# Performance work log

Hardware: AMD Instinct MI355X
Metric: run time of the kernel (lower is better)

## Reference

```python
import jax, jax.numpy as jnp
import numpy as np

BINS = 32


def _mi_from_hist(hist):
    # hist: (B, BINS, BINS) raw counts. Normalize and compute MI per sample,
    # matching np.histogram2d marginals (px from axis=1 sum, py from axis=0 sum).
    total = jnp.sum(hist, axis=(1, 2), keepdims=True)
    p = hist / total                      # joint pmf (B, BINS, BINS)
    px = jnp.sum(p, axis=2)               # (B, BINS)
    py = jnp.sum(p, axis=1)               # (B, BINS)
    denom = px[:, :, None] * py[:, None, :]
    pos = p > 0                           # p>0 implies px>0 and py>0
    ratio = jnp.where(pos, p / jnp.where(pos, denom, 1.0), 1.0)
    mi = jnp.sum(jnp.where(pos, p * jnp.log(ratio), 0.0), axis=(1, 2))
    return mi                             # (B,)


def setup_inputs() -> dict:
    key = jax.random.key(0)
    k1, k2 = jax.random.split(key)
    shape = (32, 2, 512, 512)
    return {
        "input": jax.random.normal(k1, shape, dtype=jnp.float32),
        "target": jax.random.normal(k2, shape, dtype=jnp.float32),
    }


def reference(input, target):
    B = input.shape[0]
    u = (input.reshape(B, -1) + 1.0) / 2.0   # (B, N) mapped to ~[0,1]
    v = (target.reshape(B, -1) + 1.0) / 2.0
    # np.histogram2d with range [[0,1],[0,1]] drops out-of-range points and
    # includes the right edge in the last bin.
    in_range = (u >= 0) & (u <= 1) & (v >= 0) & (v <= 1)
    w = in_range.astype(u.dtype)
    iu = jnp.clip(jnp.floor(u * BINS).astype(jnp.int32), 0, BINS - 1)
    iv = jnp.clip(jnp.floor(v * BINS).astype(jnp.int32), 0, BINS - 1)
    flat = (jnp.arange(B, dtype=jnp.int32)[:, None] * (BINS * BINS)
            + iu * BINS + iv).reshape(-1)
    hist = jax.ops.segment_sum(w.reshape(-1), flat,
                               num_segments=B * BINS * BINS)
    hist = hist.reshape(B, BINS, BINS)
    mi = _mi_from_hist(hist)
    return -jnp.mean(mi)
```

## Files before the change

### kernel.cpp

```cpp
#include <hip/hip_runtime.h>


#define BINS 32
#define NBINS2 1024
#define LDS_ROW 33
#define LDS_HIST (BINS * LDS_ROW)
#define NBATCH 32
#define N_PER_BATCH (2 * 512 * 512)
#define BLOCKS_PER_BATCH 64
#define CHUNK (N_PER_BATCH / BLOCKS_PER_BATCH)
#define THREADS 256
#define VEC_PER_THREAD (CHUNK / 4 / THREADS)

__global__ __launch_bounds__(THREADS) void zero_kernel(unsigned* __restrict__ hist,
                                                       double* __restrict__ mi,
                                                       float* __restrict__ out) {
    int i = blockIdx.x * THREADS + threadIdx.x;
    if (i < NBATCH * NBINS2) hist[i] = 0u;
    if (i < NBATCH) mi[i] = 0.0;
    if (i == 0) out[0] = 0.0f;
}

__global__ __launch_bounds__(THREADS) void hist_kernel(const float* __restrict__ x,
                                                       const float* __restrict__ y,
                                                       unsigned* __restrict__ hist) {
    __shared__ unsigned h[LDS_HIST];
    for (int i = threadIdx.x; i < LDS_HIST; i += THREADS) h[i] = 0u;
    __syncthreads();

    const int b   = blockIdx.x / BLOCKS_PER_BATCH;
    const int blk = blockIdx.x % BLOCKS_PER_BATCH;
    const long base = (long)b * N_PER_BATCH + (long)blk * CHUNK;
    const float4* xv = (const float4*)(x + base);
    const float4* yv = (const float4*)(y + base);

    float4 xa[VEC_PER_THREAD], ya[VEC_PER_THREAD];
#pragma unroll
    for (int j = 0; j < VEC_PER_THREAD; ++j) xa[j] = xv[threadIdx.x + j * THREADS];
#pragma unroll
    for (int j = 0; j < VEC_PER_THREAD; ++j) ya[j] = yv[threadIdx.x + j * THREADS];

#pragma unroll
    for (int j = 0; j < VEC_PER_THREAD; ++j) {
        float ax[4] = {xa[j].x, xa[j].y, xa[j].z, xa[j].w};
        float ty[4] = {ya[j].x, ya[j].y, ya[j].z, ya[j].w};
#pragma unroll
        for (int k = 0; k < 4; ++k) {
            float u = (ax[k] + 1.0f) * 0.5f;
            float v = (ty[k] + 1.0f) * 0.5f;
            bool ok = (u >= 0.0f) & (u <= 1.0f) & (v >= 0.0f) & (v <= 1.0f);
            if (ok) {
                int iu = (int)(u * 32.0f); if (iu > 31) iu = 31;
                int iv = (int)(v * 32.0f); if (iv > 31) iv = 31;
                atomicAdd(&h[iu * LDS_ROW + iv], 1u);
            }
        }
    }
    __syncthreads();

    unsigned* g = hist + b * NBINS2;
    for (int i = threadIdx.x; i < NBINS2; i += THREADS) {
        unsigned v = h[(i >> 5) * LDS_ROW + (i & 31)];
        if (v) atomicAdd(&g[i], v);
    }
}

__global__ __launch_bounds__(256) void mi_kernel(const unsigned* __restrict__ hist,
                                                 double* __restrict__ mi_out) {
    __shared__ unsigned c[NBINS2];
    __shared__ unsigned px[BINS];
    __shared__ unsigned py[BINS];
    __shared__ double red[4];

    const int b = blockIdx.x;
    const unsigned* g = hist + b * NBINS2;
    for (int i = threadIdx.x; i < NBINS2; i += 256) c[i] = g[i];
    __syncthreads();

    if (threadIdx.x < 32) {
        unsigned s = 0;
        for (int j = 0; j < 32; ++j) s += c[threadIdx.x * BINS + j];
        px[threadIdx.x] = s;
    } else if (threadIdx.x < 64) {
        int col = threadIdx.x - 32;
        unsigned s = 0;
        for (int j = 0; j < 32; ++j) s += c[j * BINS + col];
        py[col] = s;
    }
    __syncthreads();

    unsigned total = 0;
    for (int j = 0; j < 32; ++j) total += px[j];
    const double T = (double)total;

    double acc = 0.0;
    for (int i = threadIdx.x; i < NBINS2; i += 256) {
        unsigned cc = c[i];
        if (cc) {
            int r = i >> 5, col = i & 31;
            acc += (double)cc * log((double)cc * T / ((double)px[r] * (double)py[col]));
        }
    }
    for (int off = 32; off > 0; off >>= 1)
        acc += __shfl_down(acc, off, 64);
    int wave = threadIdx.x >> 6;
    if ((threadIdx.x & 63) == 0) red[wave] = acc;
    __syncthreads();
    if (threadIdx.x == 0) {
        double s = red[0] + red[1] + red[2] + red[3];
        mi_out[b] = s / T;
    }
}

__global__ void finalize_kernel(const double* __restrict__ mi, float* __restrict__ out) {
    if (threadIdx.x == 0) {
        double s = 0.0;
        for (int i = 0; i < NBATCH; ++i) s += mi[i];
        out[0] = (float)(-s / (double)NBATCH);
    }
}

extern "C" void kernel_launch(void* const* d_in, const int* in_sizes, int n_in,
                              void* d_out, int out_size, void* d_ws, size_t ws_size,
                              hipStream_t stream) {
    const float* x = (const float*)d_in[0];
    const float* y = (const float*)d_in[1];
    float* out = (float*)d_out;

    unsigned* hist = (unsigned*)d_ws;
    double* mi = (double*)((char*)d_ws + NBATCH * NBINS2 * sizeof(unsigned));

    zero_kernel<<<(NBATCH * NBINS2 + THREADS - 1) / THREADS, THREADS, 0, stream>>>(hist, mi, out);
    hist_kernel<<<NBATCH * BLOCKS_PER_BATCH, THREADS, 0, stream>>>(x, y, hist);
    mi_kernel<<<NBATCH, 256, 0, stream>>>(hist, mi);
    finalize_kernel<<<1, 64, 0, stream>>>(mi, out);
}
```

Measured before the change: 38.52 us.

## Replace global atomic histogram merge with per-block partials reduced in MI kernel

Each histogram block now writes its private LDS histogram to its own slot in a workspace partials buffer, with no global atomics. The MI kernel, launched with 1024 threads, sums the partials for each batch before computing MI. This removes the zeroing kernel launch and global atomic contention. The hist kernel is templated on blocks-per-batch and processes tiles of 8 float4 per thread, and the block count is picked from the workspace size. The trade-off is extra partial-buffer traffic, 8 MB at 64 blocks per batch, read serially in the MI kernel, and fewer blocks if the workspace is small.

```diff
diff --git a/kernel.cpp b/kernel.cpp
--- a/kernel.cpp
+++ b/kernel.cpp
@@ -7,85 +7,81 @@
 #define LDS_HIST (BINS * LDS_ROW)
 #define NBATCH 32
 #define N_PER_BATCH (2 * 512 * 512)
-#define BLOCKS_PER_BATCH 64
-#define CHUNK (N_PER_BATCH / BLOCKS_PER_BATCH)
 #define THREADS 256
-#define VEC_PER_THREAD (CHUNK / 4 / THREADS)
 
-__global__ __launch_bounds__(THREADS) void zero_kernel(unsigned* __restrict__ hist,
-                                                       double* __restrict__ mi,
-                                                       float* __restrict__ out) {
-    int i = blockIdx.x * THREADS + threadIdx.x;
-    if (i < NBATCH * NBINS2) hist[i] = 0u;
-    if (i < NBATCH) mi[i] = 0.0;
-    if (i == 0) out[0] = 0.0f;
-}
-
+template <int BPB>
 __global__ __launch_bounds__(THREADS) void hist_kernel(const float* __restrict__ x,
                                                        const float* __restrict__ y,
-                                                       unsigned* __restrict__ hist) {
+                                                       unsigned* __restrict__ parts) {
+    constexpr int CHUNKF = N_PER_BATCH / BPB;
+    constexpr int NVEC   = CHUNKF / 4;
+    constexpr int TILE   = THREADS * 8;
+    constexpr int NTILE  = NVEC / TILE;
+
     __shared__ unsigned h[LDS_HIST];
     for (int i = threadIdx.x; i < LDS_HIST; i += THREADS) h[i] = 0u;
     __syncthreads();
 
-    const int b   = blockIdx.x / BLOCKS_PER_BATCH;
-    const int blk = blockIdx.x % BLOCKS_PER_BATCH;
-    const long base = (long)b * N_PER_BATCH + (long)blk * CHUNK;
-    const float4* xv = (const float4*)(x + base);
-    const float4* yv = (const float4*)(y + base);
-
-    float4 xa[VEC_PER_THREAD], ya[VEC_PER_THREAD];
-#pragma unroll
-    for (int j = 0; j < VEC_PER_THREAD; ++j) xa[j] = xv[threadIdx.x + j * THREADS];
-#pragma unroll
-    for (int j = 0; j < VEC_PER_THREAD; ++j) ya[j] = yv[threadIdx.x + j * THREADS];
+    const float4* xv = (const float4*)x + (size_t)blockIdx.x * NVEC;
+    const float4* yv = (const float4*)y + (size_t)blockIdx.x * NVEC;
 
 #pragma unroll
-    for (int j = 0; j < VEC_PER_THREAD; ++j) {
-        float ax[4] = {xa[j].x, xa[j].y, xa[j].z, xa[j].w};
-        float ty[4] = {ya[j].x, ya[j].y, ya[j].z, ya[j].w};
+    for (int t = 0; t < NTILE; ++t) {
+        float4 xa[8], ya[8];
 #pragma unroll
-        for (int k = 0; k < 4; ++k) {
-            float u = (ax[k] + 1.0f) * 0.5f;
-            float v = (ty[k] + 1.0f) * 0.5f;
-            bool ok = (u >= 0.0f) & (u <= 1.0f) & (v >= 0.0f) & (v <= 1.0f);
-            if (ok) {
-                int iu = (int)(u * 32.0f); if (iu > 31) iu = 31;
-                int iv = (int)(v * 32.0f); if (iv > 31) iv = 31;
-                atomicAdd(&h[iu * LDS_ROW + iv], 1u);
+        for (int j = 0; j < 8; ++j) xa[j] = xv[t * TILE + j * THREADS + threadIdx.x];
+#pragma unroll
+        for (int j = 0; j < 8; ++j) ya[j] = yv[t * TILE + j * THREADS + threadIdx.x];
+
+#pragma unroll
+        for (int j = 0; j < 8; ++j) {
+            float ax[4] = {xa[j].x, xa[j].y, xa[j].z, xa[j].w};
+            float ty[4] = {ya[j].x, ya[j].y, ya[j].z, ya[j].w};
+#pragma unroll
+            for (int k = 0; k < 4; ++k) {
+                float u = (ax[k] + 1.0f) * 0.5f;
+                float v = (ty[k] + 1.0f) * 0.5f;
+                bool ok = (u >= 0.0f) & (u <= 1.0f) & (v >= 0.0f) & (v <= 1.0f);
+                if (ok) {
+                    int iu = (int)(u * 32.0f); if (iu > 31) iu = 31;
+                    int iv = (int)(v * 32.0f); if (iv > 31) iv = 31;
+                    atomicAdd(&h[iu * LDS_ROW + iv], 1u);
+                }
             }
         }
     }
     __syncthreads();
 
-    unsigned* g = hist + b * NBINS2;
-    for (int i = threadIdx.x; i < NBINS2; i += THREADS) {
-        unsigned v = h[(i >> 5) * LDS_ROW + (i & 31)];
-        if (v) atomicAdd(&g[i], v);
-    }
+    unsigned* g = parts + (size_t)blockIdx.x * NBINS2;
+    for (int i = threadIdx.x; i < NBINS2; i += THREADS)
+        g[i] = h[(i >> 5) * LDS_ROW + (i & 31)];
 }
 
-__global__ __launch_bounds__(256) void mi_kernel(const unsigned* __restrict__ hist,
-                                                 double* __restrict__ mi_out) {
+__global__ __launch_bounds__(1024) void mi_kernel(const unsigned* __restrict__ parts,
+                                                  int nparts,
+                                                  double* __restrict__ mi_out) {
     __shared__ unsigned c[NBINS2];
     __shared__ unsigned px[BINS];
     __shared__ unsigned py[BINS];
-    __shared__ double red[4];
+    __shared__ double red[16];
 
     const int b = blockIdx.x;
-    const unsigned* g = hist + b * NBINS2;
-    for (int i = threadIdx.x; i < NBINS2; i += 256) c[i] = g[i];
+    const unsigned* base = parts + (size_t)b * nparts * NBINS2 + threadIdx.x;
+    unsigned s = 0;
+#pragma unroll 8
+    for (int p = 0; p < nparts; ++p) s += base[(size_t)p * NBINS2];
+    c[threadIdx.x] = s;
     __syncthreads();
 
     if (threadIdx.x < 32) {
-        unsigned s = 0;
-        for (int j = 0; j < 32; ++j) s += c[threadIdx.x * BINS + j];
-        px[threadIdx.x] = s;
+        unsigned r = 0;
+        for (int j = 0; j < 32; ++j) r += c[threadIdx.x * BINS + j];
+        px[threadIdx.x] = r;
     } else if (threadIdx.x < 64) {
         int col = threadIdx.x - 32;
-        unsigned s = 0;
-        for (int j = 0; j < 32; ++j) s += c[j * BINS + col];
-        py[col] = s;
+        unsigned r = 0;
+        for (int j = 0; j < 32; ++j) r += c[j * BINS + col];
+        py[col] = r;
     }
     __syncthreads();
 
@@ -94,11 +90,11 @@
     const double T = (double)total;
 
     double acc = 0.0;
-    for (int i = threadIdx.x; i < NBINS2; i += 256) {
-        unsigned cc = c[i];
+    {
+        unsigned cc = c[threadIdx.x];
         if (cc) {
-            int r = i >> 5, col = i & 31;
-            acc += (double)cc * log((double)cc * T / ((double)px[r] * (double)py[col]));
+            int r = threadIdx.x >> 5, col = threadIdx.x & 31;
+            acc = (double)cc * log((double)cc * T / ((double)px[r] * (double)py[col]));
         }
     }
     for (int off = 32; off > 0; off >>= 1)
@@ -107,8 +103,9 @@
     if ((threadIdx.x & 63) == 0) red[wave] = acc;
     __syncthreads();
     if (threadIdx.x == 0) {
-        double s = red[0] + red[1] + red[2] + red[3];
-        mi_out[b] = s / T;
+        double t = 0.0;
+        for (int i = 0; i < 16; ++i) t += red[i];
+        mi_out[b] = t / T;
     }
 }
 
@@ -127,11 +124,20 @@
     const float* y = (const float*)d_in[1];
     float* out = (float*)d_out;
 
-    unsigned* hist = (unsigned*)d_ws;
-    double* mi = (double*)((char*)d_ws + NBATCH * NBINS2 * sizeof(unsigned));
+    unsigned* parts = (unsigned*)d_ws;
 
-    zero_kernel<<<(NBATCH * NBINS2 + THREADS - 1) / THREADS, THREADS, 0, stream>>>(hist, mi, out);
-    hist_kernel<<<NBATCH * BLOCKS_PER_BATCH, THREADS, 0, stream>>>(x, y, hist);
-    mi_kernel<<<NBATCH, 256, 0, stream>>>(hist, mi);
+    int bpb;
+    if (ws_size >= (size_t)NBATCH * 64 * NBINS2 * sizeof(unsigned) + 256) bpb = 64;
+    else if (ws_size >= (size_t)NBATCH * 16 * NBINS2 * sizeof(unsigned) + 256) bpb = 16;
+    else bpb = 4;
+
+    double* mi = (double*)((char*)d_ws + (size_t)NBATCH * bpb * NBINS2 * sizeof(unsigned));
+
+    switch (bpb) {
+        case 64: hist_kernel<64><<<NBATCH * 64, THREADS, 0, stream>>>(x, y, parts); break;
+        case 16: hist_kernel<16><<<NBATCH * 16, THREADS, 0, stream>>>(x, y, parts); break;
+        default: hist_kernel<4><<<NBATCH * 4, THREADS, 0, stream>>>(x, y, parts); break;
+    }
+    mi_kernel<<<NBATCH, 1024, 0, stream>>>(parts, bpb, mi);
     finalize_kernel<<<1, 64, 0, stream>>>(mi, out);
 }
```

After: 35.65 us. 7.5% less time.
